# Optimization experiments

Hardware: AMD Instinct MI355X
Metric: run time of the kernel (lower is better)

Reference implementation:

```python
import jax, jax.numpy as jnp
import numpy as np

IN_DIM = 128
LAYER_DIMS = [128, 128]
NUM_SAMPLES = [25, 10]
L0 = 3072
NEG_WEIGHT = 1.0


def setup_inputs() -> dict:
    key = jax.random.key(0)
    ks = jax.random.split(key, 12)
    feat = jax.random.normal(ks[0], (L0, IN_DIM), dtype=jnp.float32)
    nodes = jax.random.randint(ks[1], (L0,), 0, L0)
    nb0 = jnp.arange(L0)
    nb1 = jax.random.randint(ks[2], (L0 * 10,), 0, L0)
    nb2 = jax.random.randint(ks[3], (L0 * 10 * 25,), 0, L0)
    src_idx = jax.random.randint(ks[4], (1024,), 0, L0)
    pos_idx = jax.random.randint(ks[5], (1024,), 0, L0)
    neg_idx = jax.random.randint(ks[6], (512,), 0, L0)
    g = 0.05
    # mean aggregator weights: layer0 in=IN_DIM, layer1 in=2*128 (concat)
    w_self_0 = jax.random.normal(ks[7], (IN_DIM, 128), jnp.float32) * g
    w_neigh_0 = jax.random.normal(ks[8], (IN_DIM, 128), jnp.float32) * g
    w_self_1 = jax.random.normal(ks[9], (256, 128), jnp.float32) * g
    w_neigh_1 = jax.random.normal(ks[10], (256, 128), jnp.float32) * g
    return dict(nodes=nodes, feat=feat, src_idx=src_idx, pos_idx=pos_idx,
                neg_idx=neg_idx, nb0=nb0, nb1=nb1, nb2=nb2,
                w_self_0=w_self_0, w_neigh_0=w_neigh_0,
                w_self_1=w_self_1, w_neigh_1=w_neigh_1)


def _aggregate(hidden, params):
    # GraphSAGE layer stack: at layer l, combine each hop with the mean of its
    # sampled neighbors, concat self/neigh transforms, relu except last layer.
    num_layers = len(NUM_SAMPLES)
    for layer in range(num_layers):
        w_self, w_neigh = params[layer]
        is_last = layer == num_layers - 1
        next_hidden = []
        for hop in range(num_layers - layer):
            s = NUM_SAMPLES[num_layers - hop - 1]
            self_v = hidden[hop]  # [n, d]
            neigh = hidden[hop + 1].reshape(self_v.shape[0], s, self_v.shape[1])
            neigh_mean = jnp.mean(neigh, axis=1)
            h = jnp.concatenate([self_v @ w_self, neigh_mean @ w_neigh], axis=1)
            if not is_last:
                h = jax.nn.relu(h)
            next_hidden.append(h)
        hidden = next_hidden
    return hidden[0]


def _l2_normalize(x, eps=1e-12):
    return x * jax.lax.rsqrt(jnp.maximum(jnp.sum(x * x, axis=1, keepdims=True), eps))


def reference(nodes, feat, src_idx, pos_idx, neg_idx, nb0, nb1, nb2,
              w_self_0, w_neigh_0, w_self_1, w_neigh_1):
    hidden = [feat[nb0], feat[nb1], feat[nb2]]
    params = [(w_self_0, w_neigh_0), (w_self_1, w_neigh_1)]
    output = _aggregate(hidden, params)          # [L0, 256]
    output = _l2_normalize(output)
    src_emb = output[src_idx]                    # [B, 256]
    pos_emb = output[pos_idx]
    neg_emb = output[neg_idx]                    # [Nneg, 256]

    aff = jnp.sum(src_emb * pos_emb, axis=1)     # [B]
    neg_aff = src_emb @ neg_emb.T                # [B, Nneg]

    # MRR via double argsort (tf double top_k equivalent; ties -> positive last)
    aff_all = jnp.concatenate([neg_aff, aff[:, None]], axis=1)
    order = jnp.argsort(-aff_all, axis=1, stable=True)
    ranks = jnp.argsort(order, axis=1, stable=True)
    mrr = jnp.mean(1.0 / (ranks[:, -1].astype(jnp.float32) + 1.0))

    # sigmoid cross-entropy: labels 1 -> softplus(-x); labels 0 -> softplus(x)
    true_xent = jax.nn.softplus(-aff)
    neg_xent = jax.nn.softplus(neg_aff)
    loss = jnp.sum(true_xent) + NEG_WEIGHT * jnp.sum(neg_xent)
    loss = loss / jnp.asarray(src_emb.shape[0], jnp.float32)
    return src_emb, loss, mrr
```

## Files before the change

### kernel.cpp

```cpp
#include <hip/hip_runtime.h>
#include <math.h>

#define L0      3072
#define BATCH   1024
#define NNEG    512


__device__ __forceinline__ float bf2f(unsigned short u) {
  return __uint_as_float(((unsigned)u) << 16);
}
__device__ __forceinline__ void store_out(float v, float* p) { *p = v; }
__device__ __forceinline__ void store_out(float v, unsigned short* p) {
  unsigned x = __float_as_uint(v);
  *p = (unsigned short)((x + 0x7fff + ((x >> 16) & 1)) >> 16);
}

template<int K, int AW, int HOFF, bool NORM, typename OutT>
__global__ __launch_bounds__(512) void k_mm(
    const float* __restrict__ Ain,
    const float* __restrict__ W0, const float* __restrict__ W1,
    OutT* __restrict__ Out, const int ldo, const int outHalfOff,
    float* __restrict__ zbuf, const int zcount) {
  __shared__ float AT[6 * AW];
  __shared__ float rs[8][3];
  const int t = threadIdx.x;
  if (zbuf != nullptr && blockIdx.x == 0)
    for (int z = t; z < zcount; z += 512) zbuf[z] = 0.f;
  const int base = blockIdx.x * 6;
  {
    const float4* __restrict__ src = (const float4*)(Ain + base * AW);
    float4* __restrict__ dst = (float4*)AT;
    for (int idx = t; idx < 6 * AW / 4; idx += 512) dst[idx] = src[idx];
  }
  __syncthreads();

  const int wave = t >> 6;
  const int half = wave >> 2;
  const int colg = (wave >> 1) & 1;
  const int rowg = wave & 1;
  const int rg = rowg * 3;
  const int col = colg * 64 + (t & 63);
  const float* __restrict__ W = (half ? W1 : W0) + col;
  const float* __restrict__ A0 = AT + rg * AW + half * HOFF;

  float acc[3] = {0.f, 0.f, 0.f};
#pragma unroll 4
  for (int d = 0; d < K; d += 4) {
    float4 a[3];
#pragma unroll
    for (int r = 0; r < 3; ++r) a[r] = *(const float4*)&A0[r * AW + d];
    float w[4];
#pragma unroll
    for (int i2 = 0; i2 < 4; ++i2) w[i2] = W[(d + i2) * 128];
#pragma unroll
    for (int i2 = 0; i2 < 4; ++i2)
#pragma unroll
      for (int r = 0; r < 3; ++r)
        acc[r] = fmaf(((const float*)&a[r])[i2], w[i2], acc[r]);
  }

  float scale[3] = {1.f, 1.f, 1.f};
  if (NORM) {
    float p[3];
#pragma unroll
    for (int r = 0; r < 3; ++r) p[r] = acc[r] * acc[r];
#pragma unroll
    for (int off = 32; off > 0; off >>= 1)
#pragma unroll
      for (int r = 0; r < 3; ++r) p[r] += __shfl_xor(p[r], off, 64);
    if ((t & 63) == 0) { rs[wave][0] = p[0]; rs[wave][1] = p[1]; rs[wave][2] = p[2]; }
    __syncthreads();
#pragma unroll
    for (int r = 0; r < 3; ++r) {
      const float s = rs[rowg][r] + rs[rowg + 2][r] + rs[rowg + 4][r] + rs[rowg + 6][r];
      scale[r] = rsqrtf(fmaxf(s, 1e-12f));
    }
  }
  OutT* __restrict__ O = Out + half * outHalfOff;
#pragma unroll
  for (int r = 0; r < 3; ++r)
    store_out(acc[r] * scale[r], &O[(base + rg + r) * ldo + col]);
}

__global__ __launch_bounds__(640) void k_aggregate(
    const unsigned short* __restrict__ X0, const unsigned short* __restrict__ Y0,
    const int* __restrict__ nb0, const int* __restrict__ nb1,
    const int* __restrict__ nb2, float* __restrict__ H) {
  __shared__ float gB[10][128], gC[10][128], gD[10][128];
  const int i = blockIdx.x;
  const int t = threadIdx.x;
  const int n0 = nb0[i];
  const int j = t >> 6;
  const int lam = t & 63;
  const int r = i * 10 + j;
  int myidx = 0;
  if (lam < 25) myidx = nb2[r * 25 + lam];
  else if (lam == 25) myidx = nb1[r];
  const int c8 = lam & 15;
  const int sub = lam >> 4;

  float d8[8];
#pragma unroll
  for (int e = 0; e < 8; ++e) d8[e] = 0.f;
#pragma unroll
  for (int m = 0; m < 7; ++m) {
    const int k = sub + 4 * m;
    const int ridx = __shfl(myidx, k, 64);
    if (k < 25) {
      const float4 raw = *(const float4*)(Y0 + ridx * 128 + c8 * 8);
      const unsigned short* u = (const unsigned short*)&raw;
#pragma unroll
      for (int e = 0; e < 8; ++e) d8[e] += bf2f(u[e]);
    }
  }
#pragma unroll
  for (int e = 0; e < 8; ++e) d8[e] += __shfl_xor(d8[e], 16, 64);
#pragma unroll
  for (int e = 0; e < 8; ++e) d8[e] += __shfl_xor(d8[e], 32, 64);

  const int r1 = __shfl(myidx, 25, 64);
  if (sub == 0) {
#pragma unroll
    for (int e = 0; e < 8; ++e) gD[j][c8 * 8 + e] = fmaxf(d8[e] * 0.04f, 0.f);
    const float4 raw = *(const float4*)(Y0 + r1 * 128 + c8 * 8);
    const unsigned short* u = (const unsigned short*)&raw;
#pragma unroll
    for (int e = 0; e < 8; ++e) gB[j][c8 * 8 + e] = bf2f(u[e]);
  } else if (sub == 1) {
    const float4 raw = *(const float4*)(X0 + r1 * 128 + c8 * 8);
    const unsigned short* u = (const unsigned short*)&raw;
#pragma unroll
    for (int e = 0; e < 8; ++e) gC[j][c8 * 8 + e] = fmaxf(bf2f(u[e]), 0.f);
  }
  __syncthreads();

  if (t < 512) {
    const int q = t >> 7, c = t & 127;
    float v;
    if (q == 0) {
      v = fmaxf(bf2f(X0[n0 * 128 + c]), 0.f);
    } else {
      const float* g = (q == 1) ? &gB[0][0] : (q == 2) ? &gC[0][0] : &gD[0][0];
      float s = 0.f;
#pragma unroll
      for (int jj = 0; jj < 10; ++jj) s += g[jj * 128 + c];
      v = s * 0.1f;
      if (q == 1) v = fmaxf(v, 0.f);
    }
    H[i * 512 + t] = v;
  }
}

__device__ __forceinline__ float softplusf(float x) {
  return fmaxf(x, 0.f) + log1pf(expf(-fabsf(x)));
}

__global__ __launch_bounds__(256) void k_neg(
    const float* __restrict__ O, const int* __restrict__ src_idx,
    const int* __restrict__ pos_idx, const int* __restrict__ neg_idx,
    float* __restrict__ out_src, int* __restrict__ rank,
    float* __restrict__ spPos, float* __restrict__ spNeg) {
  __shared__ float SL[32][129];
  __shared__ float NL[64][129];
  __shared__ float affL[32];
  __shared__ int cntL[32];
  const int t = threadIdx.x;
  const int rowBase = (blockIdx.x >> 3) * 32;
  const int colBase = (blockIdx.x & 7) * 64;
  const bool first = (colBase == 0);
  if (t < 32) {
    const int b = rowBase + t;
    const float* __restrict__ ps = O + src_idx[b] * 256;
    const float* __restrict__ pp = O + pos_idx[b] * 256;
    float a = 0.f;
#pragma unroll 16
    for (int d = 0; d < 256; ++d) a = fmaf(ps[d], pp[d], a);
    affL[t] = a;
    cntL[t] = 0;
    if (first) atomicAdd(spPos, softplusf(-a));
  }
  if (first) {
    for (int idx = t; idx < 32 * 64; idx += 256) {
      const int rr = idx >> 6, qq = idx & 63;
      ((float4*)out_src)[(rowBase + rr) * 64 + qq] =
          ((const float4*)O)[src_idx[rowBase + rr] * 64 + qq];
    }
  }
  const int ct = t & 31;
  const int rt = t >> 5;
  float acc[4][2];
#pragma unroll
  for (int k = 0; k < 4; ++k) { acc[k][0] = 0.f; acc[k][1] = 0.f; }
  for (int ch = 0; ch < 2; ++ch) {
    __syncthreads();
    for (int idx = t; idx < 32 * 128; idx += 256) {
      int r = idx >> 7, dd = idx & 127;
      SL[r][dd] = O[src_idx[rowBase + r] * 256 + ch * 128 + dd];
    }
    for (int idx = t; idx < 64 * 128; idx += 256) {
      int cpos = idx >> 7, dd = idx & 127;
      NL[cpos][dd] = O[neg_idx[colBase + cpos] * 256 + ch * 128 + dd];
    }
    __syncthreads();
    for (int dd = 0; dd < 128; ++dd) {
      float n0 = NL[ct][dd], n1 = NL[ct + 32][dd];
#pragma unroll
      for (int k = 0; k < 4; ++k) {
        float sv = SL[rt + 8 * k][dd];
        acc[k][0] = fmaf(sv, n0, acc[k][0]);
        acc[k][1] = fmaf(sv, n1, acc[k][1]);
      }
    }
  }
  float sp = 0.f;
#pragma unroll
  for (int k = 0; k < 4; ++k) {
    float a = affL[rt + 8 * k];
    int cnt = 0;
#pragma unroll
    for (int cc = 0; cc < 2; ++cc) {
      float v = acc[k][cc];
      sp += softplusf(v);
      cnt += (v >= a) ? 1 : 0;
    }
    if (cnt) atomicAdd(&cntL[rt + 8 * k], cnt);
  }
#pragma unroll
  for (int off = 32; off > 0; off >>= 1) sp += __shfl_down(sp, off, 64);
  if ((t & 63) == 0) atomicAdd(spNeg, sp);
  __syncthreads();
  if (t < 32) atomicAdd(&rank[rowBase + t], cntL[t]);
}

__global__ __launch_bounds__(256) void k_finalize(
    const int* __restrict__ rank, const float* __restrict__ spPos,
    const float* __restrict__ spNeg, float* __restrict__ out) {
  const int t = threadIdx.x;
  float s = 0.f;
  for (int i = t; i < BATCH; i += 256) s += 1.f / (float)(rank[i] + 1);
#pragma unroll
  for (int off = 32; off > 0; off >>= 1) s += __shfl_down(s, off, 64);
  __shared__ float wsum[4];
  if ((t & 63) == 0) wsum[t >> 6] = s;
  __syncthreads();
  if (t == 0) {
    float mrr = (wsum[0] + wsum[1] + wsum[2] + wsum[3]) * (1.f / 1024.f);
    float loss = (spPos[0] + spNeg[0]) * (1.f / 1024.f);
    out[BATCH * 256]     = loss;
    out[BATCH * 256 + 1] = mrr;
  }
}

extern "C" void kernel_launch(void* const* d_in, const int* in_sizes, int n_in,
                              void* d_out, int out_size, void* d_ws, size_t ws_size,
                              hipStream_t stream) {
  const float* feat   = (const float*)d_in[1];
  const int* src_idx  = (const int*)d_in[2];
  const int* pos_idx  = (const int*)d_in[3];
  const int* neg_idx  = (const int*)d_in[4];
  const int* nb0      = (const int*)d_in[5];
  const int* nb1      = (const int*)d_in[6];
  const int* nb2      = (const int*)d_in[7];
  const float* ws0    = (const float*)d_in[8];
  const float* wn0    = (const float*)d_in[9];
  const float* ws1    = (const float*)d_in[10];
  const float* wn1    = (const float*)d_in[11];

  float* wsf = (float*)d_ws;
  unsigned short* X0 = (unsigned short*)d_ws;
  unsigned short* Y0 = X0 + 393216;
  float* H     = wsf + 393216;
  float* R     = wsf + 1966080;
  float* spPos = wsf + 2752512;
  float* spNeg = wsf + 2752513;
  int*   rank  = (int*)(wsf + 2752514);
  float* out   = (float*)d_out;

  k_mm<128, 128, 0, false, unsigned short><<<L0 / 6, 512, 0, stream>>>(
      feat, ws0, wn0, X0, 128, 393216, spPos, 1026);
  k_aggregate<<<L0, 640, 0, stream>>>(X0, Y0, nb0, nb1, nb2, H);
  k_mm<256, 512, 256, true, float><<<L0 / 6, 512, 0, stream>>>(
      H, ws1, wn1, R, 256, 128, nullptr, 0);
  k_neg<<<(BATCH / 32) * (NNEG / 64), 256, 0, stream>>>(
      R, src_idx, pos_idx, neg_idx, out, rank, spPos, spNeg);
  k_finalize<<<1, 256, 0, stream>>>(rank, spPos, spNeg, out);
}
```

Measured before the change: 165.4 us.

## Retile negative-affinity kernel to 32x32 tiles with full-depth float4 LDS loads

```diff
diff --git a/kernel.cpp b/kernel.cpp
--- a/kernel.cpp
+++ b/kernel.cpp
@@ -160,14 +160,24 @@
     const int* __restrict__ pos_idx, const int* __restrict__ neg_idx,
     float* __restrict__ out_src, int* __restrict__ rank,
     float* __restrict__ spPos, float* __restrict__ spNeg) {
-  __shared__ float SL[32][129];
-  __shared__ float NL[64][129];
+  __shared__ float S[32][260];
+  __shared__ float N[32][260];
   __shared__ float affL[32];
-  __shared__ int cntL[32];
-  const int t = threadIdx.x;
-  const int rowBase = (blockIdx.x >> 3) * 32;
-  const int colBase = (blockIdx.x & 7) * 64;
+  const int t = threadIdx.x;
+  const int rowBase = (blockIdx.x >> 4) * 32;
+  const int colBase = (blockIdx.x & 15) * 32;
   const bool first = (colBase == 0);
+
+  for (int idx = t; idx < 64 * 64; idx += 256) {
+    const int row = idx >> 6, q = idx & 63;
+    if (row < 32) {
+      *(float4*)&S[row][q * 4] =
+          ((const float4*)O)[src_idx[rowBase + row] * 64 + q];
+    } else {
+      *(float4*)&N[row - 32][q * 4] =
+          ((const float4*)O)[neg_idx[colBase + row - 32] * 64 + q];
+    }
+  }
   if (t < 32) {
     const int b = rowBase + t;
     const float* __restrict__ ps = O + src_idx[b] * 256;
@@ -176,7 +186,6 @@
 #pragma unroll 16
     for (int d = 0; d < 256; ++d) a = fmaf(ps[d], pp[d], a);
     affL[t] = a;
-    cntL[t] = 0;
     if (first) atomicAdd(spPos, softplusf(-a));
   }
   if (first) {
@@ -186,50 +195,43 @@
           ((const float4*)O)[src_idx[rowBase + rr] * 64 + qq];
     }
   }
-  const int ct = t & 31;
-  const int rt = t >> 5;
-  float acc[4][2];
-#pragma unroll
-  for (int k = 0; k < 4; ++k) { acc[k][0] = 0.f; acc[k][1] = 0.f; }
-  for (int ch = 0; ch < 2; ++ch) {
-    __syncthreads();
-    for (int idx = t; idx < 32 * 128; idx += 256) {
-      int r = idx >> 7, dd = idx & 127;
-      SL[r][dd] = O[src_idx[rowBase + r] * 256 + ch * 128 + dd];
-    }
-    for (int idx = t; idx < 64 * 128; idx += 256) {
-      int cpos = idx >> 7, dd = idx & 127;
-      NL[cpos][dd] = O[neg_idx[colBase + cpos] * 256 + ch * 128 + dd];
-    }
-    __syncthreads();
-    for (int dd = 0; dd < 128; ++dd) {
-      float n0 = NL[ct][dd], n1 = NL[ct + 32][dd];
-#pragma unroll
-      for (int k = 0; k < 4; ++k) {
-        float sv = SL[rt + 8 * k][dd];
-        acc[k][0] = fmaf(sv, n0, acc[k][0]);
-        acc[k][1] = fmaf(sv, n1, acc[k][1]);
-      }
-    }
-  }
-  float sp = 0.f;
-#pragma unroll
-  for (int k = 0; k < 4; ++k) {
-    float a = affL[rt + 8 * k];
-    int cnt = 0;
-#pragma unroll
-    for (int cc = 0; cc < 2; ++cc) {
-      float v = acc[k][cc];
-      sp += softplusf(v);
-      cnt += (v >= a) ? 1 : 0;
-    }
-    if (cnt) atomicAdd(&cntL[rt + 8 * k], cnt);
-  }
+  __syncthreads();
+
+  const int r2 = t >> 4, c2 = t & 15;
+  float a00 = 0.f, a01 = 0.f, a10 = 0.f, a11 = 0.f;
+  for (int dd = 0; dd < 256; dd += 4) {
+    const float4 s0 = *(const float4*)&S[r2][dd];
+    const float4 s1 = *(const float4*)&S[r2 + 16][dd];
+    const float4 n0 = *(const float4*)&N[c2][dd];
+    const float4 n1 = *(const float4*)&N[c2 + 16][dd];
+#pragma unroll
+    for (int e = 0; e < 4; ++e) {
+      const float se0 = ((const float*)&s0)[e], se1 = ((const float*)&s1)[e];
+      const float ne0 = ((const float*)&n0)[e], ne1 = ((const float*)&n1)[e];
+      a00 = fmaf(se0, ne0, a00);
+      a01 = fmaf(se0, ne1, a01);
+      a10 = fmaf(se1, ne0, a10);
+      a11 = fmaf(se1, ne1, a11);
+    }
+  }
+
+  float sp = softplusf(a00) + softplusf(a01) + softplusf(a10) + softplusf(a11);
 #pragma unroll
   for (int off = 32; off > 0; off >>= 1) sp += __shfl_down(sp, off, 64);
   if ((t & 63) == 0) atomicAdd(spNeg, sp);
-  __syncthreads();
-  if (t < 32) atomicAdd(&rank[rowBase + t], cntL[t]);
+
+  const float af0 = affL[r2], af1 = affL[r2 + 16];
+  int c0 = (a00 >= af0 ? 1 : 0) + (a01 >= af0 ? 1 : 0);
+  int c1 = (a10 >= af1 ? 1 : 0) + (a11 >= af1 ? 1 : 0);
+#pragma unroll
+  for (int off = 8; off > 0; off >>= 1) {
+    c0 += __shfl_down(c0, off, 16);
+    c1 += __shfl_down(c1, off, 16);
+  }
+  if (c2 == 0) {
+    if (c0) atomicAdd(&rank[rowBase + r2], c0);
+    if (c1) atomicAdd(&rank[rowBase + r2 + 16], c1);
+  }
 }
 
 __global__ __launch_bounds__(256) void k_finalize(
@@ -281,7 +283,7 @@
   k_aggregate<<<L0, 640, 0, stream>>>(X0, Y0, nb0, nb1, nb2, H);
   k_mm<256, 512, 256, true, float><<<L0 / 6, 512, 0, stream>>>(
       H, ws1, wn1, R, 256, 128, nullptr, 0);
-  k_neg<<<(BATCH / 32) * (NNEG / 64), 256, 0, stream>>>(
+  k_neg<<<512, 256, 0, stream>>>(
       R, src_idx, pos_idx, neg_idx, out, rank, spPos, spNeg);
   k_finalize<<<1, 256, 0, stream>>>(rank, spPos, spNeg, out);
 }
```

Result: slower. 174.5 us (+5.5%).

## Use bf16 MFMA for negative affinities and split positive-affinity kernel

Applied to the files above, without the earlier changes.

```diff
diff --git a/kernel.cpp b/kernel.cpp
--- a/kernel.cpp
+++ b/kernel.cpp
@@ -4,6 +4,10 @@
 #define L0      3072
 #define BATCH   1024
 #define NNEG    512
+#define LDP     264
+
+typedef __attribute__((ext_vector_type(8))) short bf16x8;
+typedef __attribute__((ext_vector_type(4))) float f32x4;
 
 
 __device__ __forceinline__ float bf2f(unsigned short u) {
@@ -20,6 +24,7 @@
     const float* __restrict__ Ain,
     const float* __restrict__ W0, const float* __restrict__ W1,
     OutT* __restrict__ Out, const int ldo, const int outHalfOff,
+    unsigned short* __restrict__ OutB,
     float* __restrict__ zbuf, const int zcount) {
   __shared__ float AT[6 * AW];
   __shared__ float rs[8][3];
@@ -78,8 +83,12 @@
   }
   OutT* __restrict__ O = Out + half * outHalfOff;
 #pragma unroll
-  for (int r = 0; r < 3; ++r)
-    store_out(acc[r] * scale[r], &O[(base + rg + r) * ldo + col]);
+  for (int r = 0; r < 3; ++r) {
+    const float v = acc[r] * scale[r];
+    store_out(v, &O[(base + rg + r) * ldo + col]);
+    if (OutB != nullptr)
+      store_out(v, &OutB[(base + rg + r) * 256 + half * 128 + col]);
+  }
 }
 
 __global__ __launch_bounds__(640) void k_aggregate(
@@ -155,81 +164,100 @@
   return fmaxf(x, 0.f) + log1pf(expf(-fabsf(x)));
 }
 
+__global__ __launch_bounds__(64) void k_aff(
+    const unsigned short* __restrict__ Rb, const float* __restrict__ R,
+    const int* __restrict__ src_idx, const int* __restrict__ pos_idx,
+    float* __restrict__ out_src, float* __restrict__ aff,
+    float* __restrict__ spPos) {
+  __shared__ unsigned short Sb[16][LDP];
+  __shared__ unsigned short Pb[16][LDP];
+  const int t = threadIdx.x;
+  const int rowBase = blockIdx.x * 16;
+  for (int idx = t; idx < 32 * 32; idx += 64) {
+    const int row = idx >> 5, q = idx & 31;
+    const int gr = (row < 16) ? src_idx[rowBase + row] : pos_idx[rowBase + row - 16];
+    const float4 v = ((const float4*)(Rb + gr * 256))[q];
+    unsigned short* dst = (row < 16) ? &Sb[row][0] : &Pb[row - 16][0];
+    *(float4*)(dst + q * 8) = v;
+  }
+  for (int idx = t; idx < 16 * 64; idx += 64) {
+    const int row = idx >> 6, q = idx & 63;
+    ((float4*)out_src)[(rowBase + row) * 64 + q] =
+        ((const float4*)(R + src_idx[rowBase + row] * 256))[q];
+  }
+  __syncthreads();
+  const int lm = t & 15, quad = t >> 4;
+  const unsigned short* Sp = &Sb[lm][quad * 8];
+  const unsigned short* Pp = &Pb[lm][quad * 8];
+  f32x4 d = {0.f, 0.f, 0.f, 0.f};
+#pragma unroll
+  for (int k0 = 0; k0 < 256; k0 += 32) {
+    bf16x8 a = *(const bf16x8*)(Sp + k0);
+    bf16x8 b = *(const bf16x8*)(Pp + k0);
+    d = __builtin_amdgcn_mfma_f32_16x16x32_bf16(a, b, d, 0, 0, 0);
+  }
+#pragma unroll
+  for (int j = 0; j < 4; ++j) {
+    const int row = quad * 4 + j;
+    if (lm == row) {
+      aff[rowBase + row] = d[j];
+      atomicAdd(spPos, softplusf(-d[j]));
+    }
+  }
+}
+
 __global__ __launch_bounds__(256) void k_neg(
-    const float* __restrict__ O, const int* __restrict__ src_idx,
-    const int* __restrict__ pos_idx, const int* __restrict__ neg_idx,
-    float* __restrict__ out_src, int* __restrict__ rank,
-    float* __restrict__ spPos, float* __restrict__ spNeg) {
-  __shared__ float SL[32][129];
-  __shared__ float NL[64][129];
+    const unsigned short* __restrict__ Rb, const int* __restrict__ src_idx,
+    const int* __restrict__ neg_idx, const float* __restrict__ aff,
+    int* __restrict__ rank, float* __restrict__ spNeg) {
+  __shared__ unsigned short Sb[32][LDP];
+  __shared__ unsigned short Nb[64][LDP];
   __shared__ float affL[32];
-  __shared__ int cntL[32];
   const int t = threadIdx.x;
   const int rowBase = (blockIdx.x >> 3) * 32;
   const int colBase = (blockIdx.x & 7) * 64;
-  const bool first = (colBase == 0);
-  if (t < 32) {
-    const int b = rowBase + t;
-    const float* __restrict__ ps = O + src_idx[b] * 256;
-    const float* __restrict__ pp = O + pos_idx[b] * 256;
-    float a = 0.f;
-#pragma unroll 16
-    for (int d = 0; d < 256; ++d) a = fmaf(ps[d], pp[d], a);
-    affL[t] = a;
-    cntL[t] = 0;
-    if (first) atomicAdd(spPos, softplusf(-a));
-  }
-  if (first) {
-    for (int idx = t; idx < 32 * 64; idx += 256) {
-      const int rr = idx >> 6, qq = idx & 63;
-      ((float4*)out_src)[(rowBase + rr) * 64 + qq] =
-          ((const float4*)O)[src_idx[rowBase + rr] * 64 + qq];
-    }
-  }
-  const int ct = t & 31;
-  const int rt = t >> 5;
-  float acc[4][2];
-#pragma unroll
-  for (int k = 0; k < 4; ++k) { acc[k][0] = 0.f; acc[k][1] = 0.f; }
-  for (int ch = 0; ch < 2; ++ch) {
-    __syncthreads();
-    for (int idx = t; idx < 32 * 128; idx += 256) {
-      int r = idx >> 7, dd = idx & 127;
-      SL[r][dd] = O[src_idx[rowBase + r] * 256 + ch * 128 + dd];
-    }
-    for (int idx = t; idx < 64 * 128; idx += 256) {
-      int cpos = idx >> 7, dd = idx & 127;
-      NL[cpos][dd] = O[neg_idx[colBase + cpos] * 256 + ch * 128 + dd];
-    }
-    __syncthreads();
-    for (int dd = 0; dd < 128; ++dd) {
-      float n0 = NL[ct][dd], n1 = NL[ct + 32][dd];
-#pragma unroll
-      for (int k = 0; k < 4; ++k) {
-        float sv = SL[rt + 8 * k][dd];
-        acc[k][0] = fmaf(sv, n0, acc[k][0]);
-        acc[k][1] = fmaf(sv, n1, acc[k][1]);
-      }
-    }
-  }
+  if (t < 32) affL[t] = aff[rowBase + t];
+  for (int idx = t; idx < 96 * 32; idx += 256) {
+    const int row = idx >> 5, q = idx & 31;
+    const int gr = (row < 32) ? src_idx[rowBase + row]
+                              : neg_idx[colBase + row - 32];
+    const float4 v = ((const float4*)(Rb + gr * 256))[q];
+    unsigned short* dst = (row < 32) ? &Sb[row][0] : &Nb[row - 32][0];
+    *(float4*)(dst + q * 8) = v;
+  }
+  __syncthreads();
+
+  const int l = t & 63, w = t >> 6;
+  const int mt = w & 1, np = w >> 1;
+  const int lm = l & 15, quad = l >> 4;
+  const unsigned short* Sp = &Sb[mt * 16 + lm][quad * 8];
+  const unsigned short* N0 = &Nb[np * 32 + lm][quad * 8];
+  const unsigned short* N1 = &Nb[np * 32 + 16 + lm][quad * 8];
+  f32x4 d0 = {0.f, 0.f, 0.f, 0.f}, d1 = {0.f, 0.f, 0.f, 0.f};
+#pragma unroll
+  for (int k0 = 0; k0 < 256; k0 += 32) {
+    bf16x8 a = *(const bf16x8*)(Sp + k0);
+    bf16x8 b0 = *(const bf16x8*)(N0 + k0);
+    bf16x8 b1 = *(const bf16x8*)(N1 + k0);
+    d0 = __builtin_amdgcn_mfma_f32_16x16x32_bf16(a, b0, d0, 0, 0, 0);
+    d1 = __builtin_amdgcn_mfma_f32_16x16x32_bf16(a, b1, d1, 0, 0, 0);
+  }
+
   float sp = 0.f;
 #pragma unroll
-  for (int k = 0; k < 4; ++k) {
-    float a = affL[rt + 8 * k];
-    int cnt = 0;
-#pragma unroll
-    for (int cc = 0; cc < 2; ++cc) {
-      float v = acc[k][cc];
-      sp += softplusf(v);
-      cnt += (v >= a) ? 1 : 0;
-    }
-    if (cnt) atomicAdd(&cntL[rt + 8 * k], cnt);
+  for (int j = 0; j < 4; ++j) {
+    const int row = mt * 16 + quad * 4 + j;
+    const float a = affL[row];
+    const float v0 = d0[j], v1 = d1[j];
+    sp += softplusf(v0) + softplusf(v1);
+    int c = (v0 >= a ? 1 : 0) + (v1 >= a ? 1 : 0);
+#pragma unroll
+    for (int off = 8; off > 0; off >>= 1) c += __shfl_down(c, off, 16);
+    if (lm == 0 && c) atomicAdd(&rank[rowBase + row], c);
   }
 #pragma unroll
   for (int off = 32; off > 0; off >>= 1) sp += __shfl_down(sp, off, 64);
-  if ((t & 63) == 0) atomicAdd(spNeg, sp);
-  __syncthreads();
-  if (t < 32) atomicAdd(&rank[rowBase + t], cntL[t]);
+  if (l == 0) atomicAdd(spNeg, sp);
 }
 
 __global__ __launch_bounds__(256) void k_finalize(
@@ -271,17 +299,20 @@
   unsigned short* Y0 = X0 + 393216;
   float* H     = wsf + 393216;
   float* R     = wsf + 1966080;
-  float* spPos = wsf + 2752512;
-  float* spNeg = wsf + 2752513;
-  int*   rank  = (int*)(wsf + 2752514);
+  unsigned short* Rb = (unsigned short*)(wsf + 2752512);
+  float* aff   = wsf + 3145728;
+  float* spPos = wsf + 3146752;
+  float* spNeg = wsf + 3146753;
+  int*   rank  = (int*)(wsf + 3146754);
   float* out   = (float*)d_out;
 
   k_mm<128, 128, 0, false, unsigned short><<<L0 / 6, 512, 0, stream>>>(
-      feat, ws0, wn0, X0, 128, 393216, spPos, 1026);
+      feat, ws0, wn0, X0, 128, 393216, nullptr, spPos, 1026);
   k_aggregate<<<L0, 640, 0, stream>>>(X0, Y0, nb0, nb1, nb2, H);
   k_mm<256, 512, 256, true, float><<<L0 / 6, 512, 0, stream>>>(
-      H, ws1, wn1, R, 256, 128, nullptr, 0);
+      H, ws1, wn1, R, 256, 128, Rb, nullptr, 0);
+  k_aff<<<BATCH / 16, 64, 0, stream>>>(Rb, R, src_idx, pos_idx, out, aff, spPos);
   k_neg<<<(BATCH / 32) * (NNEG / 64), 256, 0, stream>>>(
-      R, src_idx, pos_idx, neg_idx, out, rank, spPos, spNeg);
+      Rb, src_idx, neg_idx, aff, rank, spNeg);
   k_finalize<<<1, 256, 0, stream>>>(rank, spPos, spNeg, out);
 }
```

Result: no change. 166.2 us (+0.4%).
